# Optimization experiments

Measured on AMD Instinct MI355X. Metric: run time of the kernel, lower is better.

Reference implementation:

```python
import jax, jax.numpy as jnp
import numpy as np

FP8_MAX = 448.0   # max normal of float8_e4m3fn
BLOCK = 128       # block_size
EPS = 1e-12


def setup_inputs() -> dict:
    key = jax.random.key(0)
    k1, k2 = jax.random.split(key)
    M, K, N = 8192, 2048, 2048  # tokens, in_features, out_features
    x = jax.random.normal(k1, (M, K), dtype=jnp.float32)
    # Build an fp8 blockwise-quantized weight (as the module stores it):
    w = jax.random.normal(k2, (N, K), dtype=jnp.float32) * 0.02
    wb = w.reshape(N // BLOCK, BLOCK, K // BLOCK, BLOCK)
    amax = jnp.max(jnp.abs(wb), axis=(1, 3))                      # [Nb, Kb]
    w_scale = jnp.maximum(amax, EPS) / FP8_MAX                    # fp32 per-block scale
    w_q = (wb / w_scale[:, None, :, None]).astype(jnp.float8_e4m3fn)
    weight = w_q.reshape(N, K)                                    # fp8 [N, K]
    return {"x": x, "weight": weight, "w_scale": w_scale}


def reference(x, weight, w_scale):
    M, K = x.shape
    N = weight.shape[0]
    # --- fp8_blockwise_act_quant: per (1, BLOCK) block along last dim ---
    xb = x.reshape(M, K // BLOCK, BLOCK)
    amax = jnp.max(jnp.abs(xb), axis=-1)                          # [M, Kb]
    x_scale = jnp.maximum(amax, EPS) / FP8_MAX                    # [M, Kb]
    x_q = (xb / x_scale[:, :, None]).astype(jnp.float8_e4m3fn).astype(jnp.float32)
    # --- blockwise_fp8_gemm: y[m,n] = sum_kb (xq_blk . wq_blk) * xs[m,kb] * ws[nb,kb]
    # Scales factor per-block, so dequantize then a single GEMM is exactly equivalent.
    x_deq = (x_q * x_scale[:, :, None]).reshape(M, K)             # [M, K]
    ws_full = jnp.repeat(jnp.repeat(w_scale, BLOCK, axis=0), BLOCK, axis=1)  # [N, K]
    w_deq = weight.astype(jnp.float32) * ws_full                  # [N, K]
    y = x_deq @ w_deq.T                                           # [M, N]
    return y
```

## Files before the change

kernel.cpp:

```cpp
#include <hip/hip_runtime.h>
#include <cstdint>
#include <cstddef>

#define MDIM 8192
#define KDIM 2048
#define NDIM 2048
#define QBLK 128
#define KB   (KDIM / QBLK)
#define NB   (NDIM / QBLK)

typedef float floatx4 __attribute__((ext_vector_type(4)));
typedef int   int4v   __attribute__((ext_vector_type(4)));
typedef int   int8v   __attribute__((ext_vector_type(8)));

#define AS1 __attribute__((address_space(1)))
#define AS3 __attribute__((address_space(3)))

__device__ inline unsigned e4m3_encode(float r) {
    unsigned u = __float_as_uint(r);
    unsigned s = (u >> 24) & 0x80u;
    float a = fabsf(r);
    if (a < 0.015625f) return s | (unsigned)(a * 512.0f + 0.25f);
    unsigned e = ((u >> 23) & 0xFFu) - 120u;
    unsigned m = (u >> 20) & 7u;
    return s | (e << 3) | m;
}

__device__ inline int is_expbyte(unsigned b) {
    unsigned e = b & 0x7Fu;
    return (e >= 0x3Bu && e <= 0x43u) || e == 0x00u;
}

#define XQ_OFF  0
#define WQ_OFF  ((size_t)MDIM * KDIM)
#define XS_OFF  (WQ_OFF + (size_t)NDIM * KDIM)

#define QXB ((MDIM * KB) / 16)
#define DWB ((NDIM * KDIM / 8) / 256)

__global__ __launch_bounds__(256) void prep_kernel(const float* __restrict__ x,
                                                   const void* __restrict__ wq,
                                                   unsigned char* __restrict__ xq,
                                                   unsigned char* __restrict__ wq8,
                                                   float* __restrict__ xs) {
    const int tid = threadIdx.x;

    if (blockIdx.x < QXB) {
        const int g = tid >> 4;
        const int l = tid & 15;
        const size_t bi = (size_t)blockIdx.x * 16 + g;
        const size_t base = bi << 7;

        const float4* xp = (const float4*)(x + base + (size_t)l * 8);
        const float4 v0 = xp[0], v1 = xp[1];
        float a = fmaxf(fmaxf(fmaxf(fabsf(v0.x), fabsf(v0.y)), fmaxf(fabsf(v0.z), fabsf(v0.w))),
                        fmaxf(fmaxf(fabsf(v1.x), fabsf(v1.y)), fmaxf(fabsf(v1.z), fabsf(v1.w))));
        a = fmaxf(a, __shfl_xor(a, 1));
        a = fmaxf(a, __shfl_xor(a, 2));
        a = fmaxf(a, __shfl_xor(a, 4));
        a = fmaxf(a, __shfl_xor(a, 8));

        const float scale = fmaxf(a, 1e-12f) / 448.0f;
        if (l == 0) xs[bi] = scale;

        const float q0 = v0.x / scale, q1 = v0.y / scale, q2 = v0.z / scale, q3 = v0.w / scale;
        const float q4 = v1.x / scale, q5 = v1.y / scale, q6 = v1.z / scale, q7 = v1.w / scale;
        int w0 = __builtin_amdgcn_cvt_pk_fp8_f32(q0, q1, 0, false);
        w0 = __builtin_amdgcn_cvt_pk_fp8_f32(q2, q3, w0, true);
        int w1 = __builtin_amdgcn_cvt_pk_fp8_f32(q4, q5, 0, false);
        w1 = __builtin_amdgcn_cvt_pk_fp8_f32(q6, q7, w1, true);
        *(uint2*)(xq + base + (size_t)l * 8) = make_uint2((unsigned)w0, (unsigned)w1);
    } else {
        const int lane = tid & 63;
        const unsigned pw = ((const unsigned*)wq)[lane];
        const unsigned long long m3 = __ballot(is_expbyte((pw >> 24) & 0xFFu));
        const unsigned long long m1 = __ballot(((pw >> 8) & 0xFFu) == 0u);
        const int f = (__popcll(m3) >= 56) ? ((__popcll(m1) >= 56) ? 2 : 1) : 0;

        const size_t idx = (size_t)(blockIdx.x - QXB) * 256 + tid;
        const size_t off = idx * 8;

        unsigned lo, hi;
        if (f == 2) {
            const float4* p = (const float4*)((const float*)wq + off);
            const float4 a = p[0], b = p[1];
            lo = e4m3_encode(a.x) | (e4m3_encode(a.y) << 8) | (e4m3_encode(a.z) << 16) | (e4m3_encode(a.w) << 24);
            hi = e4m3_encode(b.x) | (e4m3_encode(b.y) << 8) | (e4m3_encode(b.z) << 16) | (e4m3_encode(b.w) << 24);
        } else if (f == 1) {
            const ushort4 h0 = *(const ushort4*)((const unsigned short*)wq + off);
            const ushort4 h1 = *(((const ushort4*)((const unsigned short*)wq + off)) + 1);
            lo = e4m3_encode(__uint_as_float((unsigned)h0.x << 16))
               | (e4m3_encode(__uint_as_float((unsigned)h0.y << 16)) << 8)
               | (e4m3_encode(__uint_as_float((unsigned)h0.z << 16)) << 16)
               | (e4m3_encode(__uint_as_float((unsigned)h0.w << 16)) << 24);
            hi = e4m3_encode(__uint_as_float((unsigned)h1.x << 16))
               | (e4m3_encode(__uint_as_float((unsigned)h1.y << 16)) << 8)
               | (e4m3_encode(__uint_as_float((unsigned)h1.z << 16)) << 16)
               | (e4m3_encode(__uint_as_float((unsigned)h1.w << 16)) << 24);
        } else {
            const uint2 d = *(const uint2*)((const unsigned char*)wq + off);
            lo = d.x; hi = d.y;
        }
        *(uint2*)(wq8 + off) = make_uint2(lo, hi);
    }
}

__global__ __launch_bounds__(256, 4) void gemm_mx_kernel(const unsigned char* __restrict__ Aq,
                                                         const unsigned char* __restrict__ Bq,
                                                         const float* __restrict__ xs,
                                                         const float* __restrict__ wsc,
                                                         float* __restrict__ C) {
    __shared__ unsigned char sA[128 * 128];
    __shared__ unsigned char sB[128 * 128];
    __shared__ float sxs[KB][128];

    const int tid  = threadIdx.x;
    const int wave = tid >> 6;
    const int lane = tid & 63;
    const int lrow = lane & 15;
    const int lk   = lane >> 4;
    const int lk4  = lk * 4;
    const int wm   = (wave & 1) * 64;
    const int wn   = (wave >> 1) * 64;
    const int m0   = blockIdx.y * 128;
    const int n0   = blockIdx.x * 128;
    const int nb   = n0 >> 7;

    const int srow = tid >> 3;
    const int gck  = (tid & 7) ^ (srow & 7);
    const unsigned char* agp = Aq + (size_t)(m0 + srow) * KDIM + gck * 16;
    const unsigned char* bgp = Bq + (size_t)(n0 + srow) * KDIM + gck * 16;

    if (tid < 128) {
        const float4* xp = (const float4*)(xs + (size_t)(m0 + tid) * KB);
        const float* wp = wsc + nb * KB;
#pragma unroll
        for (int q = 0; q < 4; ++q) {
            const float4 v = xp[q];
            sxs[q * 4 + 0][tid] = v.x * wp[q * 4 + 0];
            sxs[q * 4 + 1][tid] = v.y * wp[q * 4 + 1];
            sxs[q * 4 + 2][tid] = v.z * wp[q * 4 + 2];
            sxs[q * 4 + 3][tid] = v.w * wp[q * 4 + 3];
        }
    }

    floatx4 acc[4][4] = {};
    const floatx4 zero = {0.f, 0.f, 0.f, 0.f};

    for (int kb = 0; kb < KB; ++kb) {
        const size_t koff = (size_t)kb * QBLK;
        __syncthreads();
#pragma unroll
        for (int it = 0; it < 4; ++it)
            __builtin_amdgcn_global_load_lds(
                (const AS1 void*)(agp + (size_t)(it * 32) * KDIM + koff),
                (AS3 void*)(sA + tid * 16 + it * 4096), 16, 0, 0);
#pragma unroll
        for (int it = 0; it < 4; ++it)
            __builtin_amdgcn_global_load_lds(
                (const AS1 void*)(bgp + (size_t)(it * 32) * KDIM + koff),
                (AS3 void*)(sB + tid * 16 + it * 4096), 16, 0, 0);
        __syncthreads();

        int8v bf[4];
#pragma unroll
        for (int j = 0; j < 4; ++j) {
            const int Rb = wn + j * 16 + lrow;
            const int d0 = (lk * 2) ^ (Rb & 7);
            const int d1 = (lk * 2 + 1) ^ (Rb & 7);
            int4v blo = *(const int4v*)(sB + Rb * 128 + d0 * 16);
            int4v bhi = *(const int4v*)(sB + Rb * 128 + d1 * 16);
            bf[j] = __builtin_shufflevector(blo, bhi, 0, 1, 2, 3, 4, 5, 6, 7);
        }

#pragma unroll
        for (int i = 0; i < 4; ++i) {
            const int Ra = wm + i * 16 + lrow;
            const int c0 = (lk * 2) ^ (Ra & 7);
            const int c1 = (lk * 2 + 1) ^ (Ra & 7);
            int4v alo = *(const int4v*)(sA + Ra * 128 + c0 * 16);
            int4v ahi = *(const int4v*)(sA + Ra * 128 + c1 * 16);
            int8v af = __builtin_shufflevector(alo, ahi, 0, 1, 2, 3, 4, 5, 6, 7);

            const floatx4 cs = *(const floatx4*)&sxs[kb][wm + i * 16 + lk4];

#pragma unroll
            for (int j = 0; j < 4; ++j) {
                floatx4 blk = __builtin_amdgcn_mfma_scale_f32_16x16x128_f8f6f4(
                    af, bf[j], zero, 0, 0, 0, 0x7F7F7F7F, 0, 0x7F7F7F7F);
#pragma unroll
                for (int r = 0; r < 4; ++r)
                    acc[i][j][r] += cs[r] * blk[r];
            }
        }
    }

#pragma unroll
    for (int i = 0; i < 4; ++i) {
        const int row0 = m0 + wm + i * 16 + lk4;
#pragma unroll
        for (int r = 0; r < 4; ++r) {
            float* cp = C + (size_t)(row0 + r) * NDIM + n0 + wn + lrow;
#pragma unroll
            for (int j = 0; j < 4; ++j)
                cp[j * 16] = acc[i][j][r];
        }
    }
}

extern "C" void kernel_launch(void* const* d_in, const int* in_sizes, int n_in,
                              void* d_out, int out_size, void* d_ws, size_t ws_size,
                              hipStream_t stream) {
    const float* x      = (const float*)d_in[0];
    const void* wq      = d_in[1];
    const float* wscale = (const float*)d_in[2];
    float* y            = (float*)d_out;

    unsigned char* xq  = (unsigned char*)d_ws + XQ_OFF;
    unsigned char* wq8 = (unsigned char*)d_ws + WQ_OFF;
    float* xs          = (float*)((unsigned char*)d_ws + XS_OFF);

    prep_kernel<<<QXB + DWB, 256, 0, stream>>>(x, wq, xq, wq8, xs);
    gemm_mx_kernel<<<dim3(NDIM / 128, MDIM / 128), 256, 0, stream>>>(xq, wq8, xs, wscale, y);
}
```

Before: 168.0 us.

## Overlap next-tile LDS loads with MFMA compute and remap blocks per XCD

The per-tile load/compute loop is split so that the next K-block of B is loaded into shared memory while A fragments are consumed by MFMA. The next A block is then loaded while the next iteration reads B fragments. This hides part of the global-to-LDS latency without adding shared-memory buffers. The launch also becomes a 1D grid with a block-id remap, so that the 8 round-robin-dispatched block groups each cover a contiguous region of output tiles, improving L2 reuse per XCD. The remap assumes 8 dispatch groups and fixed tile counts, and the extra barriers add some sync cost.

```diff
diff --git a/kernel.cpp b/kernel.cpp
--- a/kernel.cpp
+++ b/kernel.cpp
@@ -122,15 +122,37 @@
     const int lk4  = lk * 4;
     const int wm   = (wave & 1) * 64;
     const int wn   = (wave >> 1) * 64;
-    const int m0   = blockIdx.y * 128;
-    const int n0   = blockIdx.x * 128;
-    const int nb   = n0 >> 7;
+
+    const int bid = blockIdx.x;
+    const int lid = ((bid & 7) << 7) | (bid >> 3);
+    const int m0  = (lid >> 4) * 128;
+    const int n0  = (lid & 15) * 128;
+    const int nb  = n0 >> 7;
 
     const int srow = tid >> 3;
     const int gck  = (tid & 7) ^ (srow & 7);
     const unsigned char* agp = Aq + (size_t)(m0 + srow) * KDIM + gck * 16;
     const unsigned char* bgp = Bq + (size_t)(n0 + srow) * KDIM + gck * 16;
 
+#define STAGE_A(kb_) do {                                                             \
+    const size_t koff_ = (size_t)(kb_) * QBLK;                                        \
+    _Pragma("unroll")                                                                 \
+    for (int it = 0; it < 4; ++it)                                                    \
+        __builtin_amdgcn_global_load_lds(                                             \
+            (const AS1 void*)(agp + (size_t)(it * 32) * KDIM + koff_),                \
+            (AS3 void*)(sA + tid * 16 + it * 4096), 16, 0, 0);                        \
+} while (0)
+#define STAGE_B(kb_) do {                                                             \
+    const size_t koff_ = (size_t)(kb_) * QBLK;                                        \
+    _Pragma("unroll")                                                                 \
+    for (int it = 0; it < 4; ++it)                                                    \
+        __builtin_amdgcn_global_load_lds(                                             \
+            (const AS1 void*)(bgp + (size_t)(it * 32) * KDIM + koff_),                \
+            (AS3 void*)(sB + tid * 16 + it * 4096), 16, 0, 0);                        \
+} while (0)
+
+    STAGE_B(0);
+    STAGE_A(0);
     if (tid < 128) {
         const float4* xp = (const float4*)(xs + (size_t)(m0 + tid) * KB);
         const float* wp = wsc + nb * KB;
@@ -143,25 +165,12 @@
             sxs[q * 4 + 3][tid] = v.w * wp[q * 4 + 3];
         }
     }
+    __syncthreads();
 
     floatx4 acc[4][4] = {};
     const floatx4 zero = {0.f, 0.f, 0.f, 0.f};
 
     for (int kb = 0; kb < KB; ++kb) {
-        const size_t koff = (size_t)kb * QBLK;
-        __syncthreads();
-#pragma unroll
-        for (int it = 0; it < 4; ++it)
-            __builtin_amdgcn_global_load_lds(
-                (const AS1 void*)(agp + (size_t)(it * 32) * KDIM + koff),
-                (AS3 void*)(sA + tid * 16 + it * 4096), 16, 0, 0);
-#pragma unroll
-        for (int it = 0; it < 4; ++it)
-            __builtin_amdgcn_global_load_lds(
-                (const AS1 void*)(bgp + (size_t)(it * 32) * KDIM + koff),
-                (AS3 void*)(sB + tid * 16 + it * 4096), 16, 0, 0);
-        __syncthreads();
-
         int8v bf[4];
 #pragma unroll
         for (int j = 0; j < 4; ++j) {
@@ -173,6 +182,9 @@
             bf[j] = __builtin_shufflevector(blo, bhi, 0, 1, 2, 3, 4, 5, 6, 7);
         }
 
+        __syncthreads();
+        if (kb + 1 < KB) STAGE_B(kb + 1);
+
 #pragma unroll
         for (int i = 0; i < 4; ++i) {
             const int Ra = wm + i * 16 + lrow;
@@ -193,7 +205,12 @@
                     acc[i][j][r] += cs[r] * blk[r];
             }
         }
-    }
+
+        __syncthreads();
+        if (kb + 1 < KB) STAGE_A(kb + 1);
+    }
+#undef STAGE_A
+#undef STAGE_B
 
 #pragma unroll
     for (int i = 0; i < 4; ++i) {
@@ -221,5 +238,5 @@
     float* xs          = (float*)((unsigned char*)d_ws + XS_OFF);
 
     prep_kernel<<<QXB + DWB, 256, 0, stream>>>(x, wq, xq, wq8, xs);
-    gemm_mx_kernel<<<dim3(NDIM / 128, MDIM / 128), 256, 0, stream>>>(xq, wq8, xs, wscale, y);
-}
+    gemm_mx_kernel<<<(MDIM / 128) * (NDIM / 128), 256, 0, stream>>>(xq, wq8, xs, wscale, y);
+}
```

Result: slower. 201.4 us (+19.9%).
